# Optimization experiments

Measured on AMD Instinct MI355X. Metric: run time of the kernel, lower is better.

## Reference

```python
import jax, jax.numpy as jnp
import numpy as np

B, N, D, DH = 8, 2048, 1024, 64

def setup_inputs() -> dict:
    key = jax.random.key(0)
    ks = jax.random.split(key, 4)
    s = 1.0 / np.sqrt(D)
    return {
        "x": jax.random.normal(ks[0], (B, N, D), dtype=jnp.float32),
        "Wq": jax.random.normal(ks[1], (D, DH), dtype=jnp.float32) * s,
        "bq": jnp.zeros((DH,), dtype=jnp.float32),
        "Wk": jax.random.normal(ks[2], (D, DH), dtype=jnp.float32) * s,
        "bk": jnp.zeros((DH,), dtype=jnp.float32),
        "Wv": jax.random.normal(ks[3], (D, DH), dtype=jnp.float32) * s,
        "bv": jnp.zeros((DH,), dtype=jnp.float32),
    }

def reference(x, Wq, bq, Wk, bk, Wv, bv):
    # Projections: [B,N,DH]
    Q = x @ Wq + bq
    K = x @ Wk + bk
    V = x @ Wv + bv
    sqrt_dh = jnp.sqrt(jnp.asarray(DH, dtype=x.dtype))
    # scores[b,i,j] = Q_i . K_j  (original materializes [B,N,N,DH]; GEMM is equivalent math)
    att = jnp.einsum("bid,bjd->bij", Q, K) / sqrt_dh
    # NOTE: original softmaxes over dim=1 (the query/i axis), not the usual j axis.
    att = jax.nn.softmax(att, axis=1)
    # Dropout is identity in eval mode.
    return jnp.einsum("bij,bjd->bid", att, V)
```

## Files before the change

### kernel.cpp

```cpp
#include <hip/hip_runtime.h>
#include <math.h>

#define Bn  8
#define Nn  2048
#define Dn  1024
#define DHn 64
#define PAD  72

typedef __attribute__((ext_vector_type(8))) short bf16x8;
typedef __attribute__((ext_vector_type(4))) float f32x4;

static __device__ inline short f2bf(float f) {
    unsigned u = __builtin_bit_cast(unsigned, f);
    u += 0x7FFFu + ((u >> 16) & 1u);
    return (short)(u >> 16);
}
static __device__ inline bf16x8 pack8(float4 a, float4 b) {
    bf16x8 v;
    v[0] = f2bf(a.x); v[1] = f2bf(a.y); v[2] = f2bf(a.z); v[3] = f2bf(a.w);
    v[4] = f2bf(b.x); v[5] = f2bf(b.y); v[6] = f2bf(b.z); v[7] = f2bf(b.w);
    return v;
}

__global__ __launch_bounds__(128) void wt_kernel(
    const float* __restrict__ Wq, const float* __restrict__ Wk,
    const float* __restrict__ Wv, short* __restrict__ Wtf)
{
    __shared__ float wsm[64][20];
    const int nt = blockIdx.x / 16, kt = blockIdx.x % 16;
    const int t = threadIdx.x;

    const int mat = nt >> 2;
    const float* Wm = (mat == 0) ? Wq : (mat == 1 ? Wk : Wv);
    {
        const int k = t >> 1, n8 = (t & 1) * 8;
        const float* src = &Wm[(size_t)(kt * 64 + k) * DHn + (nt & 3) * 16 + n8];
        const float4 f0 = ((const float4*)src)[0];
        const float4 f1 = ((const float4*)src)[1];
        *(float4*)&wsm[k][n8]     = f0;
        *(float4*)&wsm[k][n8 + 4] = f1;
    }
    __syncthreads();
    const int half = t >> 6, l = t & 63;
    const int c = l & 15, quad = l >> 4;
    bf16x8 o;
#pragma unroll
    for (int e = 0; e < 8; ++e) o[e] = f2bf(wsm[half * 32 + quad * 8 + e][c]);
    *(bf16x8*)&Wtf[((((size_t)nt * 16 + kt) * 2 + half) * 64 + l) * 8] = o;
}

__global__ __launch_bounds__(256) void qkv_kernel(
    const float* __restrict__ x, const short* __restrict__ Wtf,
    const float* __restrict__ bq, const float* __restrict__ bk,
    const float* __restrict__ bv,
    short* __restrict__ Qb, short* __restrict__ Kb, float* __restrict__ Vtf32)
{
    __shared__ __attribute__((aligned(16))) short xs[2][32][PAD];

    const int t = threadIdx.x;
    const int w = t >> 6, l = t & 63;
    const int c = l & 15, quad = l >> 4;
    const int ibase = blockIdx.x * 32;
    const int r0 = t >> 3, kc = t & 7;

    const float* xrow = &x[(size_t)(ibase + r0) * Dn + kc * 8];

    {
        const float4 a = ((const float4*)xrow)[0];
        const float4 b = ((const float4*)xrow)[1];
        *(bf16x8*)&xs[0][r0][kc * 8] = pack8(a, b);
    }

    float4 ra[4], rb[4];
#pragma unroll
    for (int k = 1; k <= 3; ++k) {
        ra[k] = ((const float4*)(xrow + k * 64))[0];
        rb[k] = ((const float4*)(xrow + k * 64))[1];
    }

    f32x4 acc[2][3];
#pragma unroll
    for (int mt = 0; mt < 2; ++mt)
#pragma unroll
        for (int nt = 0; nt < 3; ++nt) acc[mt][nt] = (f32x4){0.f, 0.f, 0.f, 0.f};

    __syncthreads();

#pragma unroll
    for (int kt = 0; kt < 16; ++kt) {
        const int cur = kt & 1;
        if (kt + 4 <= 15) {
            ra[kt & 3] = ((const float4*)(xrow + (kt + 4) * 64))[0];
            rb[kt & 3] = ((const float4*)(xrow + (kt + 4) * 64))[1];
        }
#pragma unroll
        for (int h = 0; h < 2; ++h) {
            const bf16x8 af0 = *(const bf16x8*)&xs[cur][c][h * 32 + quad * 8];
            const bf16x8 af1 = *(const bf16x8*)&xs[cur][16 + c][h * 32 + quad * 8];
#pragma unroll
            for (int nt = 0; nt < 3; ++nt) {
                const int ntg = w * 3 + nt;
                const bf16x8 bf = *(const bf16x8*)&Wtf[((((size_t)ntg * 16 + kt) * 2 + h) * 64 + l) * 8];
                acc[0][nt] = __builtin_amdgcn_mfma_f32_16x16x32_bf16(af0, bf, acc[0][nt], 0, 0, 0);
                acc[1][nt] = __builtin_amdgcn_mfma_f32_16x16x32_bf16(af1, bf, acc[1][nt], 0, 0, 0);
            }
        }
        if (kt < 15)
            *(bf16x8*)&xs[1 - cur][r0][kc * 8] = pack8(ra[(kt + 1) & 3], rb[(kt + 1) & 3]);
        __syncthreads();
    }

#pragma unroll
    for (int nt = 0; nt < 3; ++nt) {
        const int col = w * 48 + nt * 16 + c;
        const int mat = col >> 6, cm = col & 63;
        const float bias = (mat == 0 ? bq : (mat == 1 ? bk : bv))[cm];
#pragma unroll
        for (int mt = 0; mt < 2; ++mt) {
            if (mat == 2) {
                const int row = ibase + mt * 16 + quad * 4;
                const int b = row >> 11, i = row & (Nn - 1);
                float4 o;
                o.x = acc[mt][nt][0] + bias;
                o.y = acc[mt][nt][1] + bias;
                o.z = acc[mt][nt][2] + bias;
                o.w = acc[mt][nt][3] + bias;
                *(float4*)&Vtf32[((size_t)b * DHn + cm) * Nn + i] = o;
            } else {
                const float s = (mat == 1) ? 0.125f : 1.0f;
                short* Out = (mat == 0) ? Qb : Kb;
#pragma unroll
                for (int r = 0; r < 4; ++r)
                    Out[(size_t)(ibase + mt * 16 + quad * 4 + r) * DHn + cm] =
                        f2bf((acc[mt][nt][r] + bias) * s);
            }
        }
    }
}

__global__ __launch_bounds__(256) void colsum_kernel(
    const short* __restrict__ Qb, const short* __restrict__ Kb,
    float* __restrict__ lpart)
{
    __shared__ __attribute__((aligned(16))) short Qw[4][2][32][PAD];
    __shared__ float red[16][64];

    const int t = threadIdx.x;
    const int w = t >> 6, l = t & 63;
    const int c = l & 15, quad = l >> 4;
    const int bid = blockIdx.x;
    const int b = bid & 7, jt = (bid >> 3) & 31, s = bid >> 8;
    const int jbase = jt * 64;
    const int srow = l >> 1, scoff = (l & 1) * 32;

    bf16x8 kb[4][2];
#pragma unroll
    for (int nt = 0; nt < 4; ++nt)
#pragma unroll
        for (int kk = 0; kk < 2; ++kk)
            kb[nt][kk] = *(const bf16x8*)&Kb[((size_t)b * Nn + jbase + nt * 16 + c) * DHn
                                             + kk * 32 + quad * 8];

    const short* qbase = &Qb[((size_t)b * Nn + s * 512 + w * 128 + srow) * DHn + scoff];

#pragma unroll
    for (int k = 0; k < 4; ++k)
        *(bf16x8*)&Qw[w][0][srow][scoff + k * 8] = *(const bf16x8*)(qbase + k * 8);

    float lsum[4] = {0.f, 0.f, 0.f, 0.f};

    for (int it2 = 0; it2 < 4; ++it2) {
        const int cur = it2 & 1;
        bf16x8 p[4];
        if (it2 < 3) {
            const short* pq = qbase + (size_t)(it2 + 1) * 32 * DHn;
#pragma unroll
            for (int k = 0; k < 4; ++k) p[k] = *(const bf16x8*)(pq + k * 8);
        }
#pragma unroll
        for (int cc2 = 0; cc2 < 2; ++cc2) {
            const bf16x8 aq0 = *(const bf16x8*)&Qw[w][cur][cc2 * 16 + c][quad * 8];
            const bf16x8 aq1 = *(const bf16x8*)&Qw[w][cur][cc2 * 16 + c][32 + quad * 8];
#pragma unroll
            for (int nt = 0; nt < 4; ++nt) {
                f32x4 sv = (f32x4){0.f, 0.f, 0.f, 0.f};
                sv = __builtin_amdgcn_mfma_f32_16x16x32_bf16(aq0, kb[nt][0], sv, 0, 0, 0);
                sv = __builtin_amdgcn_mfma_f32_16x16x32_bf16(aq1, kb[nt][1], sv, 0, 0, 0);
                lsum[nt] += __expf(sv[0]) + __expf(sv[1]) + __expf(sv[2]) + __expf(sv[3]);
            }
        }
        if (it2 < 3) {
#pragma unroll
            for (int k = 0; k < 4; ++k)
                *(bf16x8*)&Qw[w][1 - cur][srow][scoff + k * 8] = p[k];
        }
    }

#pragma unroll
    for (int nt = 0; nt < 4; ++nt) red[w * 4 + quad][nt * 16 + c] = lsum[nt];
    __syncthreads();
    if (t < 64) {
        float sum = 0.f;
#pragma unroll
        for (int r = 0; r < 16; ++r) sum += red[r][t];
        lpart[((size_t)s * Bn + b) * Nn + jbase + t] = sum;
    }
}

__global__ __launch_bounds__(256) void vscale_kernel(
    const float* __restrict__ lpart, const float* __restrict__ Vtf32,
    short* __restrict__ Vt)
{
    const int idx = blockIdx.x * 256 + threadIdx.x;
    const int b = idx >> 14;
    const int d = (idx >> 8) & 63;
    const int j0 = (idx & 255) * 8;
    const size_t off = ((size_t)b * DHn + d) * Nn + j0;
    const size_t lj = (size_t)b * Nn + j0;

    const float* l0 = &lpart[lj];
    float4 sa = ((const float4*)l0)[0];
    float4 sb = ((const float4*)l0)[1];
#pragma unroll
    for (int s = 1; s < 4; ++s) {
        const float4 a = ((const float4*)(l0 + (size_t)s * Bn * Nn))[0];
        const float4 c = ((const float4*)(l0 + (size_t)s * Bn * Nn))[1];
        sa.x += a.x; sa.y += a.y; sa.z += a.z; sa.w += a.w;
        sb.x += c.x; sb.y += c.y; sb.z += c.z; sb.w += c.w;
    }
    float4 va = ((const float4*)&Vtf32[off])[0];
    float4 vb = ((const float4*)&Vtf32[off])[1];
    va.x /= sa.x; va.y /= sa.y; va.z /= sa.z; va.w /= sa.w;
    vb.x /= sb.x; vb.y /= sb.y; vb.z /= sb.z; vb.w /= sb.w;
    *(bf16x8*)&Vt[off] = pack8(va, vb);
}

__global__ __launch_bounds__(256, 4) void attnout_kernel(
    const short* __restrict__ Qb, const short* __restrict__ Kb,
    const short* __restrict__ Vt, float* __restrict__ outp)
{
    __shared__ __attribute__((aligned(16))) short Ks[2][64][PAD];
    __shared__ __attribute__((aligned(16))) short Vs[2][64][PAD];

    const int t = threadIdx.x;
    const int w = t >> 6, lane = t & 63;
    const int c = lane & 15, quad = lane >> 4;
    const int bid = blockIdx.x;
    const int b = bid & 7, it = (bid >> 3) & 31, s = bid >> 8;
    const int ibase = it * 64;
    const int r0 = t >> 2, cc = (t & 3) * 16;

    const int prb = ((c >> 2) << 3) + (c & 1) + ((c & 2) << 1);

    const size_t qrow = (size_t)b * Nn + ibase + w * 16 + c;
    const bf16x8 aq0 = *(const bf16x8*)&Qb[qrow * DHn + quad * 8];
    const bf16x8 aq1 = *(const bf16x8*)&Qb[qrow * DHn + 32 + quad * 8];

    const short* kbase = &Kb[((size_t)b * Nn + s * 512 + r0) * DHn + cc];
    const short* vbase = &Vt[((size_t)b * DHn + r0) * Nn + s * 512 + cc];

    *(bf16x8*)&Ks[0][r0][cc]     = *(const bf16x8*)kbase;
    *(bf16x8*)&Ks[0][r0][cc + 8] = *(const bf16x8*)(kbase + 8);
    *(bf16x8*)&Vs[0][r0][cc]     = *(const bf16x8*)vbase;
    *(bf16x8*)&Vs[0][r0][cc + 8] = *(const bf16x8*)(vbase + 8);

    f32x4 acc[4];
#pragma unroll
    for (int dn = 0; dn < 4; ++dn) acc[dn] = (f32x4){0.f, 0.f, 0.f, 0.f};
    __syncthreads();

#pragma unroll 2
    for (int jt2 = 0; jt2 < 8; ++jt2) {
        const int cur = jt2 & 1;
        bf16x8 pk0, pk1, pv0, pv1;
        if (jt2 < 7) {
            const short* pk = kbase + (size_t)(jt2 + 1) * 64 * DHn;
            pk0 = *(const bf16x8*)pk; pk1 = *(const bf16x8*)(pk + 8);
            const short* pv = vbase + (jt2 + 1) * 64;
            pv0 = *(const bf16x8*)pv; pv1 = *(const bf16x8*)(pv + 8);
        }

        f32x4 sv[4];
#pragma unroll
        for (int nt = 0; nt < 4; ++nt) {
            const int pr = prb + 2 * (nt & 1) + 32 * (nt >> 1);
            const bf16x8 kb0 = *(const bf16x8*)&Ks[cur][pr][quad * 8];
            const bf16x8 kb1 = *(const bf16x8*)&Ks[cur][pr][32 + quad * 8];
            f32x4 z = (f32x4){0.f, 0.f, 0.f, 0.f};
            z = __builtin_amdgcn_mfma_f32_16x16x32_bf16(kb0, aq0, z, 0, 0, 0);
            sv[nt] = __builtin_amdgcn_mfma_f32_16x16x32_bf16(kb1, aq1, z, 0, 0, 0);
        }

        bf16x8 ap_lo, ap_hi;
        ap_lo[0] = f2bf(__expf(sv[0][0])); ap_lo[1] = f2bf(__expf(sv[0][1]));
        ap_lo[2] = f2bf(__expf(sv[1][0])); ap_lo[3] = f2bf(__expf(sv[1][1]));
        ap_lo[4] = f2bf(__expf(sv[0][2])); ap_lo[5] = f2bf(__expf(sv[0][3]));
        ap_lo[6] = f2bf(__expf(sv[1][2])); ap_lo[7] = f2bf(__expf(sv[1][3]));
        ap_hi[0] = f2bf(__expf(sv[2][0])); ap_hi[1] = f2bf(__expf(sv[2][1]));
        ap_hi[2] = f2bf(__expf(sv[3][0])); ap_hi[3] = f2bf(__expf(sv[3][1]));
        ap_hi[4] = f2bf(__expf(sv[2][2])); ap_hi[5] = f2bf(__expf(sv[2][3]));
        ap_hi[6] = f2bf(__expf(sv[3][2])); ap_hi[7] = f2bf(__expf(sv[3][3]));

#pragma unroll
        for (int dn = 0; dn < 4; ++dn) {
            const bf16x8 vb0 = *(const bf16x8*)&Vs[cur][dn * 16 + c][quad * 8];
            const bf16x8 vb1 = *(const bf16x8*)&Vs[cur][dn * 16 + c][32 + quad * 8];
            acc[dn] = __builtin_amdgcn_mfma_f32_16x16x32_bf16(ap_lo, vb0, acc[dn], 0, 0, 0);
            acc[dn] = __builtin_amdgcn_mfma_f32_16x16x32_bf16(ap_hi, vb1, acc[dn], 0, 0, 0);
        }

        if (jt2 < 7) {
            *(bf16x8*)&Ks[1 - cur][r0][cc]     = pk0;
            *(bf16x8*)&Ks[1 - cur][r0][cc + 8] = pk1;
            *(bf16x8*)&Vs[1 - cur][r0][cc]     = pv0;
            *(bf16x8*)&Vs[1 - cur][r0][cc + 8] = pv1;
        }
        __syncthreads();
    }

    float* op = outp + (size_t)s * (Bn * Nn * DHn) + ((size_t)b * Nn + ibase) * DHn;
#pragma unroll
    for (int dn = 0; dn < 4; ++dn)
#pragma unroll
        for (int r = 0; r < 4; ++r)
            op[(w * 16 + quad * 4 + r) * DHn + dn * 16 + c] = acc[dn][r];
}

__global__ __launch_bounds__(256) void outreduce_kernel(
    const float* __restrict__ outp, float* __restrict__ out)
{
    const int id = blockIdx.x * 256 + threadIdx.x;
    const float4* p = (const float4*)outp;
    float4 r = p[id];
#pragma unroll
    for (int k = 1; k < 4; ++k) {
        const float4 a = p[id + (size_t)k * 262144];
        r.x += a.x; r.y += a.y; r.z += a.z; r.w += a.w;
    }
    ((float4*)out)[id] = r;
}

extern "C" void kernel_launch(void* const* d_in, const int* in_sizes, int n_in,
                              void* d_out, int out_size, void* d_ws, size_t ws_size,
                              hipStream_t stream)
{
    const float* x  = (const float*)d_in[0];
    const float* Wq = (const float*)d_in[1];
    const float* bq = (const float*)d_in[2];
    const float* Wk = (const float*)d_in[3];
    const float* bk = (const float*)d_in[4];
    const float* Wv = (const float*)d_in[5];
    const float* bv = (const float*)d_in[6];
    float* out = (float*)d_out;

    char* ws = (char*)d_ws;
    short* Qb    = (short*)(ws);
    short* Kb    = (short*)(ws + (size_t)(1 << 21));
    short* Vt    = (short*)(ws + (size_t)(2 << 21));
    short* Wtf   = (short*)(ws + (size_t)(3 << 21));
    float* lpart = (float*)(ws + (size_t)(3 << 21) + (1 << 19));
    float* Vtf32 = (float*)(ws + (size_t)(7 << 20));
    float* outp  = (float*)(ws + (size_t)(11 << 20));

    wt_kernel<<<dim3(192), dim3(128), 0, stream>>>(Wq, Wk, Wv, Wtf);
    qkv_kernel<<<dim3(512), dim3(256), 0, stream>>>(x, Wtf, bq, bk, bv, Qb, Kb, Vtf32);
    colsum_kernel<<<dim3(1024), dim3(256), 0, stream>>>(Qb, Kb, lpart);
    vscale_kernel<<<dim3(512), dim3(256), 0, stream>>>(lpart, Vtf32, Vt);
    attnout_kernel<<<dim3(1024), dim3(256), 0, stream>>>(Qb, Kb, Vt, outp);
    outreduce_kernel<<<dim3(1024), dim3(256), 0, stream>>>(outp, out);
}
```

Before: 149.9 us.

## Fuse V scaling and output reduction into attention kernel, drop split-j partials

V is now written straight to bf16 by the QKV kernel. The per-column softmax normaliser (reciprocal of summed lpart) is applied to the exp scores inside the attention kernel, which removes the separate vscale pass. The attention kernel no longer splits j four ways into global partial outputs. Each block covers 32 query rows over all 2048 keys, with two wave pairs each taking alternating 64-key tiles, and the two halves are reduced in shared memory. This drops the outreduce kernel and the fp32 partial buffers, at the cost of half as many blocks, longer serial loops and more LDS per block.

```diff
diff --git a/kernel.cpp b/kernel.cpp
--- a/kernel.cpp
+++ b/kernel.cpp
@@ -53,7 +53,7 @@
     const float* __restrict__ x, const short* __restrict__ Wtf,
     const float* __restrict__ bq, const float* __restrict__ bk,
     const float* __restrict__ bv,
-    short* __restrict__ Qb, short* __restrict__ Kb, float* __restrict__ Vtf32)
+    short* __restrict__ Qb, short* __restrict__ Kb, short* __restrict__ Vt)
 {
     __shared__ __attribute__((aligned(16))) short xs[2][32][PAD];
 
@@ -120,12 +120,12 @@
             if (mat == 2) {
                 const int row = ibase + mt * 16 + quad * 4;
                 const int b = row >> 11, i = row & (Nn - 1);
-                float4 o;
-                o.x = acc[mt][nt][0] + bias;
-                o.y = acc[mt][nt][1] + bias;
-                o.z = acc[mt][nt][2] + bias;
-                o.w = acc[mt][nt][3] + bias;
-                *(float4*)&Vtf32[((size_t)b * DHn + cm) * Nn + i] = o;
+                ushort4 o;
+                o.x = (unsigned short)f2bf(acc[mt][nt][0] + bias);
+                o.y = (unsigned short)f2bf(acc[mt][nt][1] + bias);
+                o.z = (unsigned short)f2bf(acc[mt][nt][2] + bias);
+                o.w = (unsigned short)f2bf(acc[mt][nt][3] + bias);
+                *(ushort4*)&Vt[((size_t)b * DHn + cm) * Nn + i] = o;
             } else {
                 const float s = (mat == 1) ? 0.125f : 1.0f;
                 short* Out = (mat == 0) ? Qb : Kb;
@@ -207,137 +207,135 @@
     }
 }
 
-__global__ __launch_bounds__(256) void vscale_kernel(
-    const float* __restrict__ lpart, const float* __restrict__ Vtf32,
-    short* __restrict__ Vt)
-{
-    const int idx = blockIdx.x * 256 + threadIdx.x;
-    const int b = idx >> 14;
-    const int d = (idx >> 8) & 63;
-    const int j0 = (idx & 255) * 8;
-    const size_t off = ((size_t)b * DHn + d) * Nn + j0;
-    const size_t lj = (size_t)b * Nn + j0;
-
-    const float* l0 = &lpart[lj];
-    float4 sa = ((const float4*)l0)[0];
-    float4 sb = ((const float4*)l0)[1];
-#pragma unroll
-    for (int s = 1; s < 4; ++s) {
-        const float4 a = ((const float4*)(l0 + (size_t)s * Bn * Nn))[0];
-        const float4 c = ((const float4*)(l0 + (size_t)s * Bn * Nn))[1];
-        sa.x += a.x; sa.y += a.y; sa.z += a.z; sa.w += a.w;
-        sb.x += c.x; sb.y += c.y; sb.z += c.z; sb.w += c.w;
-    }
-    float4 va = ((const float4*)&Vtf32[off])[0];
-    float4 vb = ((const float4*)&Vtf32[off])[1];
-    va.x /= sa.x; va.y /= sa.y; va.z /= sa.z; va.w /= sa.w;
-    vb.x /= sb.x; vb.y /= sb.y; vb.z /= sb.z; vb.w /= sb.w;
-    *(bf16x8*)&Vt[off] = pack8(va, vb);
-}
-
-__global__ __launch_bounds__(256, 4) void attnout_kernel(
+__global__ __launch_bounds__(256, 2) void attnout_kernel(
     const short* __restrict__ Qb, const short* __restrict__ Kb,
-    const short* __restrict__ Vt, float* __restrict__ outp)
-{
-    __shared__ __attribute__((aligned(16))) short Ks[2][64][PAD];
-    __shared__ __attribute__((aligned(16))) short Vs[2][64][PAD];
+    const short* __restrict__ Vt, const float* __restrict__ lpart,
+    float* __restrict__ out)
+{
+    __shared__ __attribute__((aligned(16))) short Ks[2][2][64][PAD];
+    __shared__ __attribute__((aligned(16))) short Vs[2][2][64][PAD];
+    __shared__ float rls[2048];
 
     const int t = threadIdx.x;
     const int w = t >> 6, lane = t & 63;
     const int c = lane & 15, quad = lane >> 4;
     const int bid = blockIdx.x;
-    const int b = bid & 7, it = (bid >> 3) & 31, s = bid >> 8;
-    const int ibase = it * 64;
-    const int r0 = t >> 2, cc = (t & 3) * 16;
+    const int b = bid & 7, it = bid >> 3;
+    const int ibase = it * 32;
+    const int isub = (w & 1) * 16;
+    const int jp = w >> 1;
 
     const int prb = ((c >> 2) << 3) + (c & 1) + ((c & 2) << 1);
 
-    const size_t qrow = (size_t)b * Nn + ibase + w * 16 + c;
+#pragma unroll
+    for (int k = 0; k < 8; ++k) {
+        const int j = k * 256 + t;
+        const size_t lj = (size_t)b * Nn + j;
+        const float lv = lpart[lj] + lpart[(size_t)Bn * Nn + lj]
+                       + lpart[2 * (size_t)Bn * Nn + lj] + lpart[3 * (size_t)Bn * Nn + lj];
+        rls[j] = 1.0f / lv;
+    }
+
+    const size_t qrow = (size_t)b * Nn + ibase + isub + c;
     const bf16x8 aq0 = *(const bf16x8*)&Qb[qrow * DHn + quad * 8];
     const bf16x8 aq1 = *(const bf16x8*)&Qb[qrow * DHn + 32 + quad * 8];
 
-    const short* kbase = &Kb[((size_t)b * Nn + s * 512 + r0) * DHn + cc];
-    const short* vbase = &Vt[((size_t)b * DHn + r0) * Nn + s * 512 + cc];
-
-    *(bf16x8*)&Ks[0][r0][cc]     = *(const bf16x8*)kbase;
-    *(bf16x8*)&Ks[0][r0][cc + 8] = *(const bf16x8*)(kbase + 8);
-    *(bf16x8*)&Vs[0][r0][cc]     = *(const bf16x8*)vbase;
-    *(bf16x8*)&Vs[0][r0][cc + 8] = *(const bf16x8*)(vbase + 8);
+    const int r0k = t >> 1, ck = (t & 1) * 32;
+    const int pk_ = r0k >> 6, rk_ = r0k & 63;
+    const int r0v = t >> 2, cv = (t & 3) * 32;
+    const int pv_ = cv >> 6, jv_ = cv & 63;
+    const short* kbase = &Kb[((size_t)b * Nn + r0k) * DHn + ck];
+    const short* vbase = &Vt[((size_t)b * DHn + r0v) * Nn + cv];
+
+#pragma unroll
+    for (int q2 = 0; q2 < 4; ++q2) {
+        *(bf16x8*)&Ks[0][pk_][rk_][ck + q2 * 8]  = *(const bf16x8*)(kbase + q2 * 8);
+        *(bf16x8*)&Vs[0][pv_][r0v][jv_ + q2 * 8] = *(const bf16x8*)(vbase + q2 * 8);
+    }
 
     f32x4 acc[4];
 #pragma unroll
     for (int dn = 0; dn < 4; ++dn) acc[dn] = (f32x4){0.f, 0.f, 0.f, 0.f};
     __syncthreads();
 
-#pragma unroll 2
-    for (int jt2 = 0; jt2 < 8; ++jt2) {
-        const int cur = jt2 & 1;
-        bf16x8 pk0, pk1, pv0, pv1;
-        if (jt2 < 7) {
-            const short* pk = kbase + (size_t)(jt2 + 1) * 64 * DHn;
-            pk0 = *(const bf16x8*)pk; pk1 = *(const bf16x8*)(pk + 8);
-            const short* pv = vbase + (jt2 + 1) * 64;
-            pv0 = *(const bf16x8*)pv; pv1 = *(const bf16x8*)(pv + 8);
-        }
-
+    for (int ss = 0; ss < 16; ++ss) {
+        const int cur = ss & 1;
+        bf16x8 nk[4], nv[4];
+        if (ss < 15) {
+            const short* nkp = kbase + (size_t)(ss + 1) * 128 * DHn;
+            const short* nvp = vbase + (ss + 1) * 128;
+#pragma unroll
+            for (int q2 = 0; q2 < 4; ++q2) {
+                nk[q2] = *(const bf16x8*)(nkp + q2 * 8);
+                nv[q2] = *(const bf16x8*)(nvp + q2 * 8);
+            }
+        }
+
+        const int jt = 2 * ss + jp;
         f32x4 sv[4];
 #pragma unroll
         for (int nt = 0; nt < 4; ++nt) {
             const int pr = prb + 2 * (nt & 1) + 32 * (nt >> 1);
-            const bf16x8 kb0 = *(const bf16x8*)&Ks[cur][pr][quad * 8];
-            const bf16x8 kb1 = *(const bf16x8*)&Ks[cur][pr][32 + quad * 8];
+            const bf16x8 kb0 = *(const bf16x8*)&Ks[cur][jp][pr][quad * 8];
+            const bf16x8 kb1 = *(const bf16x8*)&Ks[cur][jp][pr][32 + quad * 8];
             f32x4 z = (f32x4){0.f, 0.f, 0.f, 0.f};
             z = __builtin_amdgcn_mfma_f32_16x16x32_bf16(kb0, aq0, z, 0, 0, 0);
             sv[nt] = __builtin_amdgcn_mfma_f32_16x16x32_bf16(kb1, aq1, z, 0, 0, 0);
         }
 
+        const float* rlb = &rls[jt * 64 + quad * 8];
+        const float4 rl0 = *(const float4*)rlb;
+        const float4 rl1 = *(const float4*)(rlb + 4);
+        const float4 rh0 = *(const float4*)(rlb + 32);
+        const float4 rh1 = *(const float4*)(rlb + 36);
+
         bf16x8 ap_lo, ap_hi;
-        ap_lo[0] = f2bf(__expf(sv[0][0])); ap_lo[1] = f2bf(__expf(sv[0][1]));
-        ap_lo[2] = f2bf(__expf(sv[1][0])); ap_lo[3] = f2bf(__expf(sv[1][1]));
-        ap_lo[4] = f2bf(__expf(sv[0][2])); ap_lo[5] = f2bf(__expf(sv[0][3]));
-        ap_lo[6] = f2bf(__expf(sv[1][2])); ap_lo[7] = f2bf(__expf(sv[1][3]));
-        ap_hi[0] = f2bf(__expf(sv[2][0])); ap_hi[1] = f2bf(__expf(sv[2][1]));
-        ap_hi[2] = f2bf(__expf(sv[3][0])); ap_hi[3] = f2bf(__expf(sv[3][1]));
-        ap_hi[4] = f2bf(__expf(sv[2][2])); ap_hi[5] = f2bf(__expf(sv[2][3]));
-        ap_hi[6] = f2bf(__expf(sv[3][2])); ap_hi[7] = f2bf(__expf(sv[3][3]));
+        ap_lo[0] = f2bf(__expf(sv[0][0]) * rl0.x); ap_lo[1] = f2bf(__expf(sv[0][1]) * rl0.y);
+        ap_lo[2] = f2bf(__expf(sv[1][0]) * rl0.z); ap_lo[3] = f2bf(__expf(sv[1][1]) * rl0.w);
+        ap_lo[4] = f2bf(__expf(sv[0][2]) * rl1.x); ap_lo[5] = f2bf(__expf(sv[0][3]) * rl1.y);
+        ap_lo[6] = f2bf(__expf(sv[1][2]) * rl1.z); ap_lo[7] = f2bf(__expf(sv[1][3]) * rl1.w);
+        ap_hi[0] = f2bf(__expf(sv[2][0]) * rh0.x); ap_hi[1] = f2bf(__expf(sv[2][1]) * rh0.y);
+        ap_hi[2] = f2bf(__expf(sv[3][0]) * rh0.z); ap_hi[3] = f2bf(__expf(sv[3][1]) * rh0.w);
+        ap_hi[4] = f2bf(__expf(sv[2][2]) * rh1.x); ap_hi[5] = f2bf(__expf(sv[2][3]) * rh1.y);
+        ap_hi[6] = f2bf(__expf(sv[3][2]) * rh1.z); ap_hi[7] = f2bf(__expf(sv[3][3]) * rh1.w);
 
 #pragma unroll
         for (int dn = 0; dn < 4; ++dn) {
-            const bf16x8 vb0 = *(const bf16x8*)&Vs[cur][dn * 16 + c][quad * 8];
-            const bf16x8 vb1 = *(const bf16x8*)&Vs[cur][dn * 16 + c][32 + quad * 8];
+            const bf16x8 vb0 = *(const bf16x8*)&Vs[cur][jp][dn * 16 + c][quad * 8];
+            const bf16x8 vb1 = *(const bf16x8*)&Vs[cur][jp][dn * 16 + c][32 + quad * 8];
             acc[dn] = __builtin_amdgcn_mfma_f32_16x16x32_bf16(ap_lo, vb0, acc[dn], 0, 0, 0);
             acc[dn] = __builtin_amdgcn_mfma_f32_16x16x32_bf16(ap_hi, vb1, acc[dn], 0, 0, 0);
         }
 
-        if (jt2 < 7) {
-            *(bf16x8*)&Ks[1 - cur][r0][cc]     = pk0;
-            *(bf16x8*)&Ks[1 - cur][r0][cc + 8] = pk1;
-            *(bf16x8*)&Vs[1 - cur][r0][cc]     = pv0;
-            *(bf16x8*)&Vs[1 - cur][r0][cc + 8] = pv1;
+        if (ss < 15) {
+#pragma unroll
+            for (int q2 = 0; q2 < 4; ++q2) {
+                *(bf16x8*)&Ks[1 - cur][pk_][rk_][ck + q2 * 8]  = nk[q2];
+                *(bf16x8*)&Vs[1 - cur][pv_][r0v][jv_ + q2 * 8] = nv[q2];
+            }
         }
         __syncthreads();
     }
 
-    float* op = outp + (size_t)s * (Bn * Nn * DHn) + ((size_t)b * Nn + ibase) * DHn;
-#pragma unroll
-    for (int dn = 0; dn < 4; ++dn)
-#pragma unroll
-        for (int r = 0; r < 4; ++r)
-            op[(w * 16 + quad * 4 + r) * DHn + dn * 16 + c] = acc[dn][r];
-}
-
-__global__ __launch_bounds__(256) void outreduce_kernel(
-    const float* __restrict__ outp, float* __restrict__ out)
-{
-    const int id = blockIdx.x * 256 + threadIdx.x;
-    const float4* p = (const float4*)outp;
-    float4 r = p[id];
-#pragma unroll
-    for (int k = 1; k < 4; ++k) {
-        const float4 a = p[id + (size_t)k * 262144];
-        r.x += a.x; r.y += a.y; r.z += a.z; r.w += a.w;
-    }
-    ((float4*)out)[id] = r;
+    float* red = (float*)Ks;
+    if (jp == 1) {
+#pragma unroll
+        for (int dn = 0; dn < 4; ++dn)
+#pragma unroll
+            for (int r = 0; r < 4; ++r)
+                red[(isub + quad * 4 + r) * 65 + dn * 16 + c] = acc[dn][r];
+    }
+    __syncthreads();
+    if (jp == 0) {
+#pragma unroll
+        for (int dn = 0; dn < 4; ++dn)
+#pragma unroll
+            for (int r = 0; r < 4; ++r) {
+                const int row = isub + quad * 4 + r;
+                out[((size_t)b * Nn + ibase + row) * DHn + dn * 16 + c] =
+                    acc[dn][r] + red[row * 65 + dn * 16 + c];
+            }
+    }
 }
 
 extern "C" void kernel_launch(void* const* d_in, const int* in_sizes, int n_in,
@@ -359,13 +357,9 @@
     short* Vt    = (short*)(ws + (size_t)(2 << 21));
     short* Wtf   = (short*)(ws + (size_t)(3 << 21));
     float* lpart = (float*)(ws + (size_t)(3 << 21) + (1 << 19));
-    float* Vtf32 = (float*)(ws + (size_t)(7 << 20));
-    float* outp  = (float*)(ws + (size_t)(11 << 20));
 
     wt_kernel<<<dim3(192), dim3(128), 0, stream>>>(Wq, Wk, Wv, Wtf);
-    qkv_kernel<<<dim3(512), dim3(256), 0, stream>>>(x, Wtf, bq, bk, bv, Qb, Kb, Vtf32);
+    qkv_kernel<<<dim3(512), dim3(256), 0, stream>>>(x, Wtf, bq, bk, bv, Qb, Kb, Vt);
     colsum_kernel<<<dim3(1024), dim3(256), 0, stream>>>(Qb, Kb, lpart);
-    vscale_kernel<<<dim3(512), dim3(256), 0, stream>>>(lpart, Vtf32, Vt);
-    attnout_kernel<<<dim3(1024), dim3(256), 0, stream>>>(Qb, Kb, Vt, outp);
-    outreduce_kernel<<<dim3(1024), dim3(256), 0, stream>>>(outp, out);
-}
+    attnout_kernel<<<dim3(512), dim3(256), 0, stream>>>(Qb, Kb, Vt, lpart, out);
+}
```

Measured after the change: 149.7 us. About the same (-0.2%).
